# Kernel optimization log

Measured on AMD Instinct MI355X. Metric: run time of the kernel, lower is better.

## Reference

```python
import jax, jax.numpy as jnp
import numpy as np

# Default bone connections from BoneLengthLoss.__init__
BONES = np.array([(1, 2), (1, 3), (1, 4), (2, 5), (3, 6), (11, 12), (11, 13), (12, 14),
                  (13, 14), (14, 15), (15, 16), (16, 17), (12, 18), (18, 20), (20, 22),
                  (13, 19), (19, 21), (21, 23), (16, 24), (16, 25), (24, 26), (25, 26),
                  (24, 27), (27, 29), (29, 31), (25, 28), (28, 30), (30, 32), (17, 33),
                  (33, 34), (34, 35), (35, 36)], dtype=np.int32)
J1 = jnp.asarray(BONES[:, 0])
J2 = jnp.asarray(BONES[:, 1])

BATCH = 524288
NUM_KPTS = 37


def setup_inputs() -> dict:
    key = jax.random.key(0)
    k1, k2, k3 = jax.random.split(key, 3)
    pose_3d_pred = jax.random.normal(k1, (BATCH, NUM_KPTS, 3), dtype=jnp.float32)
    pose_3d_ref = jax.random.normal(k2, (BATCH, NUM_KPTS, 3), dtype=jnp.float32)
    valid_mask = jax.random.randint(k3, (BATCH, NUM_KPTS), 0, 2).astype(jnp.bool_)
    return {"pose_3d_pred": pose_3d_pred, "pose_3d_ref": pose_3d_ref,
            "valid_mask": valid_mask}


def reference(pose_3d_pred, pose_3d_ref, valid_mask):
    # Gather both endpoints of every bone: (B, n_bones, 3)
    pred_vec = pose_3d_pred[:, J2, :] - pose_3d_pred[:, J1, :]
    ref_vec = pose_3d_ref[:, J2, :] - pose_3d_ref[:, J1, :]
    pred_len = jnp.linalg.norm(pred_vec, axis=-1)  # (B, n_bones)
    ref_len = jnp.linalg.norm(ref_vec, axis=-1)    # (B, n_bones)
    # Bone is valid iff both endpoints are valid
    bone_valid = (valid_mask[:, J1] & valid_mask[:, J2]).astype(pred_len.dtype)
    # MSE over all valid (batch, bone) entries == mean over concatenated valid lengths
    sq_err = (pred_len - ref_len) ** 2
    num = jnp.sum(sq_err * bone_valid)
    den = jnp.sum(bone_valid)
    return num / den
```

## Files before the change

### kernel.cpp

```cpp
#include <hip/hip_runtime.h>


#define NKPT   37
#define ROWF   111
#define TROWS  64
#define TF4    1776
#define WF4    444
#define TMB    2368
#define TMW    592
#define WMW    148
#define BLOCK  256
#define WPB    4
#define GRID   1280

constexpr int J1[32] = {1,1,1,2,3,11,11,12,13,14,15,16,12,18,20,13,19,21,16,16,24,25,24,27,29,25,28,30,17,33,34,35};
constexpr int J2[32] = {2,3,4,5,6,12,13,14,14,15,16,17,18,20,22,19,21,23,24,25,26,26,27,29,31,28,30,32,33,34,35,36};

__device__ __forceinline__ void glds16(const void* g, void* l) {
    __builtin_amdgcn_global_load_lds(
        (const __attribute__((address_space(1))) void*)g,
        (__attribute__((address_space(3))) void*)l, 16, 0, 0);
}
__device__ __forceinline__ void glds4(const void* g, void* l) {
    __builtin_amdgcn_global_load_lds(
        (const __attribute__((address_space(1))) void*)g,
        (__attribute__((address_space(3))) void*)l, 4, 0, 0);
}

__global__ void init_detect(const unsigned int* __restrict__ mw,
                            unsigned int* __restrict__ ws) {
    const int tid = threadIdx.x;
    if (tid < 4) ws[tid] = 0u;
    __syncthreads();
    unsigned int local = 0;
    for (int i = tid; i < 1024; i += BLOCK) local |= mw[i] & 0xFFFFFF00u;
    if (__any(local != 0) && (tid & 63) == 0) atomicOr(&ws[2], 1u);
}

template <int G>
__device__ __forceinline__ void do_lens(const float* __restrict__ sp,
                                        float* __restrict__ len) {
#pragma unroll
    for (int k = 0; k < 8; ++k) {
        const int a = J1[G * 8 + k] * 3, b = J2[G * 8 + k] * 3;
        float dx = sp[b] - sp[a];
        float dy = sp[b + 1] - sp[a + 1];
        float dz = sp[b + 2] - sp[a + 2];
        len[k] = __builtin_amdgcn_sqrtf(dx * dx + dy * dy + dz * dz);
    }
}

template <int G>
__device__ __forceinline__ void do_acc(const float* __restrict__ sr,
                                       const unsigned char* __restrict__ sm,
                                       const float* __restrict__ plen,
                                       float& num, unsigned int& den) {
#pragma unroll
    for (int k = 0; k < 8; ++k) {
        const int a = J1[G * 8 + k], b = J2[G * 8 + k];
        const int a3 = a * 3, b3 = b * 3;
        float dx = sr[b3] - sr[a3];
        float dy = sr[b3 + 1] - sr[a3 + 1];
        float dz = sr[b3 + 2] - sr[a3 + 2];
        float rl = __builtin_amdgcn_sqrtf(dx * dx + dy * dy + dz * dz);
        unsigned int v = (unsigned int)(sm[a] & sm[b]);
        float d = plen[k] - rl;
        num += v ? d * d : 0.0f;
        den += v;
    }
}

__global__ __launch_bounds__(BLOCK, 5)
void bone_main(const float* __restrict__ pred, const float* __restrict__ ref,
               const void* __restrict__ mask, int B,
               unsigned int* __restrict__ ws, float* __restrict__ out) {
    __shared__ __align__(16) float4 s_pose[TF4];
    __shared__ __align__(4) unsigned char s_mask[TMB];
    __shared__ float s_rn[WPB];
    __shared__ unsigned int s_rd[WPB];

    const int tid  = threadIdx.x;
    const int wave = tid >> 6;
    const int lane = tid & 63;

    const bool mask_bytes = (ws[2] != 0);
    const int ntiles = B / TROWS;

    const float4* __restrict__ pred4 = (const float4*)pred;
    const float4* __restrict__ ref4  = (const float4*)ref;
    const unsigned int* __restrict__ mw = (const unsigned int*)mask;
    const int* __restrict__ mi = (const int*)mask;

    float4* s_pose_w = s_pose + wave * WF4;
    unsigned int* s_mask_w = (unsigned int*)s_mask;

    const float* sp_row = (const float*)s_pose + lane * ROWF;
    const unsigned char* sm_row = s_mask + lane * NKPT;

    float num = 0.0f;
    unsigned int den = 0u;

    for (int t = blockIdx.x; t < ntiles; t += GRID) {
        const float4* pb = pred4 + (size_t)t * TF4 + wave * WF4;
        const float4* rb = ref4  + (size_t)t * TF4 + wave * WF4;

        glds16(pb + lane,       s_pose_w);
        glds16(pb + 64 + lane,  s_pose_w + 64);
        glds16(pb + 128 + lane, s_pose_w + 128);
        glds16(pb + 192 + lane, s_pose_w + 192);
        glds16(pb + 256 + lane, s_pose_w + 256);
        glds16(pb + 320 + lane, s_pose_w + 320);
        if (lane < WF4 - 384)
            glds16(pb + 384 + lane, s_pose_w + 384);
        if (mask_bytes) {
            const unsigned int* mb = mw + (size_t)t * TMW + wave * WMW;
            glds4(mb + lane,      &s_mask_w[wave * WMW]);
            glds4(mb + 64 + lane, &s_mask_w[wave * WMW + 64]);
            if (lane < WMW - 128)
                glds4(mb + 128 + lane, &s_mask_w[wave * WMW + 128]);
        } else {
            const int* mb = mi + (size_t)t * TMB;
            for (int i = tid; i < TMB; i += BLOCK)
                s_mask[i] = (unsigned char)mb[i];
        }
        __syncthreads();

        float plen[8];
        switch (wave) {
            case 0: do_lens<0>(sp_row, plen); break;
            case 1: do_lens<1>(sp_row, plen); break;
            case 2: do_lens<2>(sp_row, plen); break;
            default: do_lens<3>(sp_row, plen); break;
        }
        __syncthreads();

        glds16(rb + lane,       s_pose_w);
        glds16(rb + 64 + lane,  s_pose_w + 64);
        glds16(rb + 128 + lane, s_pose_w + 128);
        glds16(rb + 192 + lane, s_pose_w + 192);
        glds16(rb + 256 + lane, s_pose_w + 256);
        glds16(rb + 320 + lane, s_pose_w + 320);
        if (lane < WF4 - 384)
            glds16(rb + 384 + lane, s_pose_w + 384);
        __syncthreads();

        switch (wave) {
            case 0: do_acc<0>(sp_row, sm_row, plen, num, den); break;
            case 1: do_acc<1>(sp_row, sm_row, plen, num, den); break;
            case 2: do_acc<2>(sp_row, sm_row, plen, num, den); break;
            default: do_acc<3>(sp_row, sm_row, plen, num, den); break;
        }
        __syncthreads();
    }

#pragma unroll
    for (int off = 32; off > 0; off >>= 1) {
        num += __shfl_down(num, off, 64);
        den += __shfl_down(den, off, 64);
    }
    if (lane == 0) { s_rn[wave] = num; s_rd[wave] = den; }
    __syncthreads();
    if (tid == 0) {
        float n = s_rn[0] + s_rn[1] + s_rn[2] + s_rn[3];
        unsigned int d = s_rd[0] + s_rd[1] + s_rd[2] + s_rd[3];
        atomicAdd((float*)&ws[0], n);
        atomicAdd(&ws[1], d);
        __threadfence();
        unsigned int prev = atomicAdd(&ws[3], 1u);
        if (prev == (unsigned int)(gridDim.x - 1)) {
            float fn = atomicAdd((float*)&ws[0], 0.0f);
            unsigned int fd = atomicAdd(&ws[1], 0u);
            out[0] = fn / (float)fd;
        }
    }
}

extern "C" void kernel_launch(void* const* d_in, const int* in_sizes, int n_in,
                              void* d_out, int out_size, void* d_ws, size_t ws_size,
                              hipStream_t stream) {
    const float* pred = (const float*)d_in[0];
    const float* ref  = (const float*)d_in[1];
    const void*  mask = d_in[2];
    const int n_mask  = in_sizes[2];
    const int B       = n_mask / NKPT;
    unsigned int* ws  = (unsigned int*)d_ws;

    init_detect<<<1, BLOCK, 0, stream>>>((const unsigned int*)mask, ws);
    bone_main<<<GRID, BLOCK, 0, stream>>>(pred, ref, mask, B, ws, (float*)d_out);
}
```

Before: 540.7 us.

## Software-pipeline pred/ref/mask staging with separate LDS buffers and vmcnt waits

Splits the shared pose buffer into separate pred and ref buffers and double-buffers the mask, so the next tile's pred and mask loads are issued while the current tile's ref is consumed. Explicit s_waitcnt vmcnt counts and raw barriers replace __syncthreads, letting in-flight global-to-LDS loads stay outstanding across phases. The grid shrinks to 512 blocks and launch bounds drop to 2 blocks per CU to fit the larger LDS footprint. This trades occupancy for per-block memory-level parallelism, and the hand-counted vmcnt values must match the number of issued loads or correctness breaks.

```diff
diff --git a/kernel.cpp b/kernel.cpp
--- a/kernel.cpp
+++ b/kernel.cpp
@@ -11,10 +11,14 @@
 #define WMW    148
 #define BLOCK  256
 #define WPB    4
-#define GRID   1280
+#define GRID   512
 
 constexpr int J1[32] = {1,1,1,2,3,11,11,12,13,14,15,16,12,18,20,13,19,21,16,16,24,25,24,27,29,25,28,30,17,33,34,35};
 constexpr int J2[32] = {2,3,4,5,6,12,13,14,14,15,16,17,18,20,22,19,21,23,24,25,26,26,27,29,31,28,30,32,33,34,35,36};
+
+#define WAITVM(N)  asm volatile("s_waitcnt vmcnt(" #N ")" ::: "memory")
+#define WAITLGKM() asm volatile("s_waitcnt lgkmcnt(0)" ::: "memory")
+#define BAR()      __builtin_amdgcn_s_barrier()
 
 __device__ __forceinline__ void glds16(const void* g, void* l) {
     __builtin_amdgcn_global_load_lds(
@@ -35,6 +39,20 @@
     unsigned int local = 0;
     for (int i = tid; i < 1024; i += BLOCK) local |= mw[i] & 0xFFFFFF00u;
     if (__any(local != 0) && (tid & 63) == 0) atomicOr(&ws[2], 1u);
+}
+
+__device__ __forceinline__ void stage_pose(const float4* __restrict__ g,
+                                           float4* l, int lane) {
+#pragma unroll
+    for (int k = 0; k < 6; ++k) glds16(g + k * 64 + lane, l + k * 64);
+    if (lane < WF4 - 384) glds16(g + 384 + lane, l + 384);
+}
+
+__device__ __forceinline__ void stage_mask(const unsigned int* __restrict__ mb,
+                                           unsigned int* md, int lane) {
+    glds4(mb + lane, md);
+    glds4(mb + 64 + lane, md + 64);
+    if (lane < WMW - 128) glds4(mb + 128 + lane, md + 128);
 }
 
 template <int G>
@@ -70,12 +88,34 @@
     }
 }
 
-__global__ __launch_bounds__(BLOCK, 5)
+__device__ __forceinline__ void lens_sw(int wave, const float* __restrict__ sp,
+                                        float* __restrict__ plen) {
+    switch (wave) {
+        case 0: do_lens<0>(sp, plen); break;
+        case 1: do_lens<1>(sp, plen); break;
+        case 2: do_lens<2>(sp, plen); break;
+        default: do_lens<3>(sp, plen); break;
+    }
+}
+__device__ __forceinline__ void acc_sw(int wave, const float* __restrict__ sr,
+                                       const unsigned char* __restrict__ sm,
+                                       const float* __restrict__ plen,
+                                       float& num, unsigned int& den) {
+    switch (wave) {
+        case 0: do_acc<0>(sr, sm, plen, num, den); break;
+        case 1: do_acc<1>(sr, sm, plen, num, den); break;
+        case 2: do_acc<2>(sr, sm, plen, num, den); break;
+        default: do_acc<3>(sr, sm, plen, num, den); break;
+    }
+}
+
+__global__ __launch_bounds__(BLOCK, 2)
 void bone_main(const float* __restrict__ pred, const float* __restrict__ ref,
                const void* __restrict__ mask, int B,
                unsigned int* __restrict__ ws, float* __restrict__ out) {
-    __shared__ __align__(16) float4 s_pose[TF4];
-    __shared__ __align__(4) unsigned char s_mask[TMB];
+    __shared__ __align__(16) float4 s_pred[TF4];
+    __shared__ __align__(16) float4 s_ref[TF4];
+    __shared__ __align__(16) unsigned int s_maskw[2][TMW];
     __shared__ float s_rn[WPB];
     __shared__ unsigned int s_rd[WPB];
 
@@ -91,66 +131,62 @@
     const unsigned int* __restrict__ mw = (const unsigned int*)mask;
     const int* __restrict__ mi = (const int*)mask;
 
-    float4* s_pose_w = s_pose + wave * WF4;
-    unsigned int* s_mask_w = (unsigned int*)s_mask;
-
-    const float* sp_row = (const float*)s_pose + lane * ROWF;
-    const unsigned char* sm_row = s_mask + lane * NKPT;
+    float4* s_predw = s_pred + wave * WF4;
+    float4* s_refw  = s_ref  + wave * WF4;
+
+    const float* sp_row = (const float*)s_pred + lane * ROWF;
+    const float* sr_row = (const float*)s_ref  + lane * ROWF;
+    const unsigned char* sm_row0 = (const unsigned char*)s_maskw[0] + lane * NKPT;
+    const unsigned char* sm_row1 = (const unsigned char*)s_maskw[1] + lane * NKPT;
 
     float num = 0.0f;
     unsigned int den = 0u;
 
-    for (int t = blockIdx.x; t < ntiles; t += GRID) {
-        const float4* pb = pred4 + (size_t)t * TF4 + wave * WF4;
-        const float4* rb = ref4  + (size_t)t * TF4 + wave * WF4;
-
-        glds16(pb + lane,       s_pose_w);
-        glds16(pb + 64 + lane,  s_pose_w + 64);
-        glds16(pb + 128 + lane, s_pose_w + 128);
-        glds16(pb + 192 + lane, s_pose_w + 192);
-        glds16(pb + 256 + lane, s_pose_w + 256);
-        glds16(pb + 320 + lane, s_pose_w + 320);
-        if (lane < WF4 - 384)
-            glds16(pb + 384 + lane, s_pose_w + 384);
-        if (mask_bytes) {
-            const unsigned int* mb = mw + (size_t)t * TMW + wave * WMW;
-            glds4(mb + lane,      &s_mask_w[wave * WMW]);
-            glds4(mb + 64 + lane, &s_mask_w[wave * WMW + 64]);
-            if (lane < WMW - 128)
-                glds4(mb + 128 + lane, &s_mask_w[wave * WMW + 128]);
-        } else {
+    if (mask_bytes) {
+        int t = blockIdx.x;
+        int par = 0;
+        if (t < ntiles) {
+            stage_pose(pred4 + (size_t)t * TF4 + wave * WF4, s_predw, lane);
+            stage_mask(mw + (size_t)t * TMW + wave * WMW,
+                       &s_maskw[0][wave * WMW], lane);
+        }
+        for (; t < ntiles; t += GRID) {
+            stage_pose(ref4 + (size_t)t * TF4 + wave * WF4, s_refw, lane);
+            WAITVM(7);
+            BAR();
+            float plen[8];
+            lens_sw(wave, sp_row, plen);
+            WAITLGKM();
+            BAR();
+            const int tn = t + GRID;
+            if (tn < ntiles) {
+                stage_pose(pred4 + (size_t)tn * TF4 + wave * WF4, s_predw, lane);
+                stage_mask(mw + (size_t)tn * TMW + wave * WMW,
+                           &s_maskw[par ^ 1][wave * WMW], lane);
+                WAITVM(10);
+            } else {
+                WAITVM(0);
+            }
+            BAR();
+            acc_sw(wave, sr_row, par ? sm_row1 : sm_row0, plen, num, den);
+            WAITLGKM();
+            BAR();
+            par ^= 1;
+        }
+    } else {
+        for (int t = blockIdx.x; t < ntiles; t += GRID) {
+            stage_pose(pred4 + (size_t)t * TF4 + wave * WF4, s_predw, lane);
+            stage_pose(ref4  + (size_t)t * TF4 + wave * WF4, s_refw,  lane);
+            unsigned char* smb = (unsigned char*)s_maskw[0];
             const int* mb = mi + (size_t)t * TMB;
             for (int i = tid; i < TMB; i += BLOCK)
-                s_mask[i] = (unsigned char)mb[i];
-        }
-        __syncthreads();
-
-        float plen[8];
-        switch (wave) {
-            case 0: do_lens<0>(sp_row, plen); break;
-            case 1: do_lens<1>(sp_row, plen); break;
-            case 2: do_lens<2>(sp_row, plen); break;
-            default: do_lens<3>(sp_row, plen); break;
-        }
-        __syncthreads();
-
-        glds16(rb + lane,       s_pose_w);
-        glds16(rb + 64 + lane,  s_pose_w + 64);
-        glds16(rb + 128 + lane, s_pose_w + 128);
-        glds16(rb + 192 + lane, s_pose_w + 192);
-        glds16(rb + 256 + lane, s_pose_w + 256);
-        glds16(rb + 320 + lane, s_pose_w + 320);
-        if (lane < WF4 - 384)
-            glds16(rb + 384 + lane, s_pose_w + 384);
-        __syncthreads();
-
-        switch (wave) {
-            case 0: do_acc<0>(sp_row, sm_row, plen, num, den); break;
-            case 1: do_acc<1>(sp_row, sm_row, plen, num, den); break;
-            case 2: do_acc<2>(sp_row, sm_row, plen, num, den); break;
-            default: do_acc<3>(sp_row, sm_row, plen, num, den); break;
-        }
-        __syncthreads();
+                smb[i] = (unsigned char)mb[i];
+            __syncthreads();
+            float plen[8];
+            lens_sw(wave, sp_row, plen);
+            acc_sw(wave, sr_row, sm_row0, plen, num, den);
+            __syncthreads();
+        }
     }
 
 #pragma unroll
```

New measurement: 538.7 us. No clear change (-0.4%).

## Register double-buffer pred/ref/mask tiles to overlap global loads with compute

Applied to the files above, without the earlier changes.

Replaces the direct global-to-LDS loads with explicit register staging. Each block holds two tiles in registers while it computes on the one already in LDS, so the loads for the next tile are in flight during compute. Pred and ref now get separate LDS buffers and are processed in one pass, dropping two barriers per tile. The grid shrinks to 512 blocks and launch bounds drop to 2 blocks per SM to make room for the large register footprint. The fallback path handles odd tile counts and int masks; the cost is heavy register pressure and reduced occupancy.

```diff
diff --git a/kernel.cpp b/kernel.cpp
--- a/kernel.cpp
+++ b/kernel.cpp
@@ -11,21 +11,13 @@
 #define WMW    148
 #define BLOCK  256
 #define WPB    4
-#define GRID   1280
+#define GRID   512
 
 constexpr int J1[32] = {1,1,1,2,3,11,11,12,13,14,15,16,12,18,20,13,19,21,16,16,24,25,24,27,29,25,28,30,17,33,34,35};
 constexpr int J2[32] = {2,3,4,5,6,12,13,14,14,15,16,17,18,20,22,19,21,23,24,25,26,26,27,29,31,28,30,32,33,34,35,36};
 
-__device__ __forceinline__ void glds16(const void* g, void* l) {
-    __builtin_amdgcn_global_load_lds(
-        (const __attribute__((address_space(1))) void*)g,
-        (__attribute__((address_space(3))) void*)l, 16, 0, 0);
-}
-__device__ __forceinline__ void glds4(const void* g, void* l) {
-    __builtin_amdgcn_global_load_lds(
-        (const __attribute__((address_space(1))) void*)g,
-        (__attribute__((address_space(3))) void*)l, 4, 0, 0);
-}
+#define LGKM0() asm volatile("s_waitcnt lgkmcnt(0)" ::: "memory")
+#define BAR()   __builtin_amdgcn_s_barrier()
 
 __global__ void init_detect(const unsigned int* __restrict__ mw,
                             unsigned int* __restrict__ ws) {
@@ -37,45 +29,105 @@
     if (__any(local != 0) && (tid & 63) == 0) atomicOr(&ws[2], 1u);
 }
 
+struct RegTile {
+    float4 p0, p1, p2, p3, p4, p5, p6;
+    float4 q0, q1, q2, q3, q4, q5, q6;
+    unsigned int m0, m1, m2;
+};
+
+__device__ __forceinline__ void ld_tile(RegTile& T,
+        const float4* __restrict__ pred4, const float4* __restrict__ ref4,
+        const unsigned int* __restrict__ mw, int t, int wave, int lane) {
+    const float4* pb = pred4 + (size_t)t * TF4 + wave * WF4 + lane;
+    const float4* qb = ref4  + (size_t)t * TF4 + wave * WF4 + lane;
+    const unsigned int* mb = mw + (size_t)t * TMW + wave * WMW + lane;
+    T.p0 = pb[0];   T.q0 = qb[0];
+    T.p1 = pb[64];  T.q1 = qb[64];
+    T.p2 = pb[128]; T.q2 = qb[128];
+    T.p3 = pb[192]; T.q3 = qb[192];
+    T.p4 = pb[256]; T.q4 = qb[256];
+    T.p5 = pb[320]; T.q5 = qb[320];
+    if (lane < WF4 - 384) { T.p6 = pb[384]; T.q6 = qb[384]; }
+    T.m0 = mb[0];
+    T.m1 = mb[64];
+    if (lane < WMW - 128) T.m2 = mb[128];
+}
+
+__device__ __forceinline__ void st_tile(const RegTile& T, float4* sp, float4* sq,
+                                        unsigned int* sm, int lane) {
+    sp[lane]       = T.p0;  sq[lane]       = T.q0;
+    sp[64 + lane]  = T.p1;  sq[64 + lane]  = T.q1;
+    sp[128 + lane] = T.p2;  sq[128 + lane] = T.q2;
+    sp[192 + lane] = T.p3;  sq[192 + lane] = T.q3;
+    sp[256 + lane] = T.p4;  sq[256 + lane] = T.q4;
+    sp[320 + lane] = T.p5;  sq[320 + lane] = T.q5;
+    if (lane < WF4 - 384) { sp[384 + lane] = T.p6; sq[384 + lane] = T.q6; }
+    sm[lane]      = T.m0;
+    sm[64 + lane] = T.m1;
+    if (lane < WMW - 128) sm[128 + lane] = T.m2;
+}
+
+__device__ __forceinline__ void ld_pose(RegTile& T,
+        const float4* __restrict__ pred4, const float4* __restrict__ ref4,
+        int t, int wave, int lane) {
+    const float4* pb = pred4 + (size_t)t * TF4 + wave * WF4 + lane;
+    const float4* qb = ref4  + (size_t)t * TF4 + wave * WF4 + lane;
+    T.p0 = pb[0];   T.q0 = qb[0];
+    T.p1 = pb[64];  T.q1 = qb[64];
+    T.p2 = pb[128]; T.q2 = qb[128];
+    T.p3 = pb[192]; T.q3 = qb[192];
+    T.p4 = pb[256]; T.q4 = qb[256];
+    T.p5 = pb[320]; T.q5 = qb[320];
+    if (lane < WF4 - 384) { T.p6 = pb[384]; T.q6 = qb[384]; }
+}
+__device__ __forceinline__ void st_pose(const RegTile& T, float4* sp, float4* sq,
+                                        int lane) {
+    sp[lane]       = T.p0;  sq[lane]       = T.q0;
+    sp[64 + lane]  = T.p1;  sq[64 + lane]  = T.q1;
+    sp[128 + lane] = T.p2;  sq[128 + lane] = T.q2;
+    sp[192 + lane] = T.p3;  sq[192 + lane] = T.q3;
+    sp[256 + lane] = T.p4;  sq[256 + lane] = T.q4;
+    sp[320 + lane] = T.p5;  sq[320 + lane] = T.q5;
+    if (lane < WF4 - 384) { sp[384 + lane] = T.p6; sq[384 + lane] = T.q6; }
+}
+
 template <int G>
-__device__ __forceinline__ void do_lens(const float* __restrict__ sp,
-                                        float* __restrict__ len) {
-#pragma unroll
-    for (int k = 0; k < 8; ++k) {
-        const int a = J1[G * 8 + k] * 3, b = J2[G * 8 + k] * 3;
-        float dx = sp[b] - sp[a];
-        float dy = sp[b + 1] - sp[a + 1];
-        float dz = sp[b + 2] - sp[a + 2];
-        len[k] = __builtin_amdgcn_sqrtf(dx * dx + dy * dy + dz * dz);
-    }
-}
-
-template <int G>
-__device__ __forceinline__ void do_acc(const float* __restrict__ sr,
-                                       const unsigned char* __restrict__ sm,
-                                       const float* __restrict__ plen,
-                                       float& num, unsigned int& den) {
+__device__ __forceinline__ void do_tile(const float* __restrict__ sp,
+                                        const float* __restrict__ sq,
+                                        const unsigned char* __restrict__ sm,
+                                        float& num, unsigned int& den) {
 #pragma unroll
     for (int k = 0; k < 8; ++k) {
         const int a = J1[G * 8 + k], b = J2[G * 8 + k];
         const int a3 = a * 3, b3 = b * 3;
-        float dx = sr[b3] - sr[a3];
-        float dy = sr[b3 + 1] - sr[a3 + 1];
-        float dz = sr[b3 + 2] - sr[a3 + 2];
-        float rl = __builtin_amdgcn_sqrtf(dx * dx + dy * dy + dz * dz);
+        float pdx = sp[b3] - sp[a3];
+        float pdy = sp[b3 + 1] - sp[a3 + 1];
+        float pdz = sp[b3 + 2] - sp[a3 + 2];
+        float qdx = sq[b3] - sq[a3];
+        float qdy = sq[b3 + 1] - sq[a3 + 1];
+        float qdz = sq[b3 + 2] - sq[a3 + 2];
+        float pl = __builtin_amdgcn_sqrtf(pdx * pdx + pdy * pdy + pdz * pdz);
+        float ql = __builtin_amdgcn_sqrtf(qdx * qdx + qdy * qdy + qdz * qdz);
         unsigned int v = (unsigned int)(sm[a] & sm[b]);
-        float d = plen[k] - rl;
+        float d = pl - ql;
         num += v ? d * d : 0.0f;
         den += v;
     }
 }
 
-__global__ __launch_bounds__(BLOCK, 5)
+#define COMPUTE() do { switch (wave) { \
+    case 0: do_tile<0>(sp_row, sq_row, sm_row, num, den); break; \
+    case 1: do_tile<1>(sp_row, sq_row, sm_row, num, den); break; \
+    case 2: do_tile<2>(sp_row, sq_row, sm_row, num, den); break; \
+    default: do_tile<3>(sp_row, sq_row, sm_row, num, den); break; } } while (0)
+
+__global__ __launch_bounds__(BLOCK, 2)
 void bone_main(const float* __restrict__ pred, const float* __restrict__ ref,
                const void* __restrict__ mask, int B,
                unsigned int* __restrict__ ws, float* __restrict__ out) {
-    __shared__ __align__(16) float4 s_pose[TF4];
-    __shared__ __align__(4) unsigned char s_mask[TMB];
+    __shared__ __align__(16) float4 s_pred[TF4];
+    __shared__ __align__(16) float4 s_ref[TF4];
+    __shared__ __align__(16) unsigned int s_maskw[TMW];
     __shared__ float s_rn[WPB];
     __shared__ unsigned int s_rd[WPB];
 
@@ -91,66 +143,62 @@
     const unsigned int* __restrict__ mw = (const unsigned int*)mask;
     const int* __restrict__ mi = (const int*)mask;
 
-    float4* s_pose_w = s_pose + wave * WF4;
-    unsigned int* s_mask_w = (unsigned int*)s_mask;
-
-    const float* sp_row = (const float*)s_pose + lane * ROWF;
-    const unsigned char* sm_row = s_mask + lane * NKPT;
+    float4* spw = s_pred + wave * WF4;
+    float4* sqw = s_ref  + wave * WF4;
+    unsigned int* smw = s_maskw + wave * WMW;
+
+    const float* sp_row = (const float*)s_pred + lane * ROWF;
+    const float* sq_row = (const float*)s_ref  + lane * ROWF;
+    const unsigned char* sm_row = (const unsigned char*)s_maskw + lane * NKPT;
 
     float num = 0.0f;
     unsigned int den = 0u;
 
-    for (int t = blockIdx.x; t < ntiles; t += GRID) {
-        const float4* pb = pred4 + (size_t)t * TF4 + wave * WF4;
-        const float4* rb = ref4  + (size_t)t * TF4 + wave * WF4;
-
-        glds16(pb + lane,       s_pose_w);
-        glds16(pb + 64 + lane,  s_pose_w + 64);
-        glds16(pb + 128 + lane, s_pose_w + 128);
-        glds16(pb + 192 + lane, s_pose_w + 192);
-        glds16(pb + 256 + lane, s_pose_w + 256);
-        glds16(pb + 320 + lane, s_pose_w + 320);
-        if (lane < WF4 - 384)
-            glds16(pb + 384 + lane, s_pose_w + 384);
-        if (mask_bytes) {
-            const unsigned int* mb = mw + (size_t)t * TMW + wave * WMW;
-            glds4(mb + lane,      &s_mask_w[wave * WMW]);
-            glds4(mb + 64 + lane, &s_mask_w[wave * WMW + 64]);
-            if (lane < WMW - 128)
-                glds4(mb + 128 + lane, &s_mask_w[wave * WMW + 128]);
-        } else {
-            const int* mb = mi + (size_t)t * TMB;
-            for (int i = tid; i < TMB; i += BLOCK)
-                s_mask[i] = (unsigned char)mb[i];
+    const int bid = blockIdx.x;
+    const int ntb = (bid < ntiles) ? (ntiles - bid + GRID - 1) / GRID : 0;
+
+    if (mask_bytes && ntb >= 2 && (ntb & 1) == 0) {
+        RegTile A, B2;
+        ld_tile(A,  pred4, ref4, mw, bid,        wave, lane);
+        ld_tile(B2, pred4, ref4, mw, bid + GRID, wave, lane);
+        st_tile(A, spw, sqw, smw, lane);
+        { int tn = bid + 2 * GRID;
+          if (tn < ntiles) ld_tile(A, pred4, ref4, mw, tn, wave, lane); }
+        LGKM0(); BAR();
+        for (int j = 0; j < ntb; j += 2) {
+            COMPUTE();
+            BAR();
+            st_tile(B2, spw, sqw, smw, lane);
+            { int tn = bid + (j + 3) * GRID;
+              if (tn < ntiles) ld_tile(B2, pred4, ref4, mw, tn, wave, lane); }
+            LGKM0(); BAR();
+            COMPUTE();
+            if (j + 2 < ntb) {
+                BAR();
+                st_tile(A, spw, sqw, smw, lane);
+                { int tn = bid + (j + 4) * GRID;
+                  if (tn < ntiles) ld_tile(A, pred4, ref4, mw, tn, wave, lane); }
+                LGKM0(); BAR();
+            }
         }
-        __syncthreads();
-
-        float plen[8];
-        switch (wave) {
-            case 0: do_lens<0>(sp_row, plen); break;
-            case 1: do_lens<1>(sp_row, plen); break;
-            case 2: do_lens<2>(sp_row, plen); break;
-            default: do_lens<3>(sp_row, plen); break;
+    } else {
+        for (int t = bid; t < ntiles; t += GRID) {
+            RegTile A;
+            ld_pose(A, pred4, ref4, t, wave, lane);
+            st_pose(A, spw, sqw, lane);
+            if (mask_bytes) {
+                for (int i = tid; i < TMW; i += BLOCK)
+                    s_maskw[i] = mw[(size_t)t * TMW + i];
+            } else {
+                unsigned char* smb = (unsigned char*)s_maskw;
+                const int* mb = mi + (size_t)t * TMB;
+                for (int i = tid; i < TMB; i += BLOCK)
+                    smb[i] = (unsigned char)mb[i];
+            }
+            __syncthreads();
+            COMPUTE();
+            __syncthreads();
         }
-        __syncthreads();
-
-        glds16(rb + lane,       s_pose_w);
-        glds16(rb + 64 + lane,  s_pose_w + 64);
-        glds16(rb + 128 + lane, s_pose_w + 128);
-        glds16(rb + 192 + lane, s_pose_w + 192);
-        glds16(rb + 256 + lane, s_pose_w + 256);
-        glds16(rb + 320 + lane, s_pose_w + 320);
-        if (lane < WF4 - 384)
-            glds16(rb + 384 + lane, s_pose_w + 384);
-        __syncthreads();
-
-        switch (wave) {
-            case 0: do_acc<0>(sp_row, sm_row, plen, num, den); break;
-            case 1: do_acc<1>(sp_row, sm_row, plen, num, den); break;
-            case 2: do_acc<2>(sp_row, sm_row, plen, num, den); break;
-            default: do_acc<3>(sp_row, sm_row, plen, num, den); break;
-        }
-        __syncthreads();
     }
 
 #pragma unroll
```

Result: slower. 625.0 us (+15.6%).

## Map one bone per lane over row pairs with per-wave LDS staging

Applied to the files above, without the earlier changes.

Replaces the block-wide 64-row tiles, which used global-to-LDS async loads and four block barriers per tile, with a wave-independent loop. Each wave loads two rows (pred and ref) into private LDS through float2 register loads, and each lane computes one bone for one row. This removes __syncthreads, the large LDS footprint and the wave-divergent per-bone switch, and raises the grid and occupancy target. In exchange, each wave issues many small loads per iteration with little memory-level parallelism, uses partial-lane loads, and depends on wave-synchronous LDS ordering without explicit barriers.

```diff
diff --git a/kernel.cpp b/kernel.cpp
--- a/kernel.cpp
+++ b/kernel.cpp
@@ -3,29 +3,13 @@
 
 #define NKPT   37
 #define ROWF   111
-#define TROWS  64
-#define TF4    1776
-#define WF4    444
-#define TMB    2368
-#define TMW    592
-#define WMW    148
 #define BLOCK  256
 #define WPB    4
-#define GRID   1280
+#define GRID   2048
+#define NWAVES (GRID * WPB)
 
-constexpr int J1[32] = {1,1,1,2,3,11,11,12,13,14,15,16,12,18,20,13,19,21,16,16,24,25,24,27,29,25,28,30,17,33,34,35};
-constexpr int J2[32] = {2,3,4,5,6,12,13,14,14,15,16,17,18,20,22,19,21,23,24,25,26,26,27,29,31,28,30,32,33,34,35,36};
-
-__device__ __forceinline__ void glds16(const void* g, void* l) {
-    __builtin_amdgcn_global_load_lds(
-        (const __attribute__((address_space(1))) void*)g,
-        (__attribute__((address_space(3))) void*)l, 16, 0, 0);
-}
-__device__ __forceinline__ void glds4(const void* g, void* l) {
-    __builtin_amdgcn_global_load_lds(
-        (const __attribute__((address_space(1))) void*)g,
-        (__attribute__((address_space(3))) void*)l, 4, 0, 0);
-}
+__device__ const unsigned char dJ1[32] = {1,1,1,2,3,11,11,12,13,14,15,16,12,18,20,13,19,21,16,16,24,25,24,27,29,25,28,30,17,33,34,35};
+__device__ const unsigned char dJ2[32] = {2,3,4,5,6,12,13,14,14,15,16,17,18,20,22,19,21,23,24,25,26,26,27,29,31,28,30,32,33,34,35,36};
 
 __global__ void init_detect(const unsigned int* __restrict__ mw,
                             unsigned int* __restrict__ ws) {
@@ -37,121 +21,94 @@
     if (__any(local != 0) && (tid & 63) == 0) atomicOr(&ws[2], 1u);
 }
 
-template <int G>
-__device__ __forceinline__ void do_lens(const float* __restrict__ sp,
-                                        float* __restrict__ len) {
-#pragma unroll
-    for (int k = 0; k < 8; ++k) {
-        const int a = J1[G * 8 + k] * 3, b = J2[G * 8 + k] * 3;
-        float dx = sp[b] - sp[a];
-        float dy = sp[b + 1] - sp[a + 1];
-        float dz = sp[b + 2] - sp[a + 2];
-        len[k] = __builtin_amdgcn_sqrtf(dx * dx + dy * dy + dz * dz);
-    }
-}
+template <bool MB>
+__device__ __forceinline__ void stream_pairs(
+        const float2* __restrict__ p2, const float2* __restrict__ q2,
+        const unsigned char* __restrict__ mb8, const int* __restrict__ mi,
+        int npairs, int gw, int lane, int laneB,
+        int o1, int o2, int moff1, int moff2,
+        float* __restrict__ sp, float* __restrict__ sq,
+        float& num, unsigned int& den) {
+    float2* sp2 = (float2*)sp;
+    float2* sq2 = (float2*)sq;
+    for (int pr = gw; pr < npairs; pr += NWAVES) {
+        const float2* pb_ = p2 + (size_t)pr * ROWF;
+        const float2* qb_ = q2 + (size_t)pr * ROWF;
+        float2 a0 = pb_[lane];
+        float2 a1 = pb_[laneB];
+        float2 b0 = qb_[lane];
+        float2 b1 = qb_[laneB];
+        unsigned int m1, m2;
+        if (MB) {
+            const unsigned char* mrow = mb8 + (size_t)pr * (2 * NKPT);
+            m1 = (unsigned int)mrow[moff1];
+            m2 = (unsigned int)mrow[moff2];
+        } else {
+            const int* mrow = mi + (size_t)pr * (2 * NKPT);
+            m1 = ((unsigned int)mrow[moff1]) & 1u;
+            m2 = ((unsigned int)mrow[moff2]) & 1u;
+        }
+        sp2[lane] = a0; sp2[laneB] = a1;
+        sq2[lane] = b0; sq2[laneB] = b1;
 
-template <int G>
-__device__ __forceinline__ void do_acc(const float* __restrict__ sr,
-                                       const unsigned char* __restrict__ sm,
-                                       const float* __restrict__ plen,
-                                       float& num, unsigned int& den) {
-#pragma unroll
-    for (int k = 0; k < 8; ++k) {
-        const int a = J1[G * 8 + k], b = J2[G * 8 + k];
-        const int a3 = a * 3, b3 = b * 3;
-        float dx = sr[b3] - sr[a3];
-        float dy = sr[b3 + 1] - sr[a3 + 1];
-        float dz = sr[b3 + 2] - sr[a3 + 2];
-        float rl = __builtin_amdgcn_sqrtf(dx * dx + dy * dy + dz * dz);
-        unsigned int v = (unsigned int)(sm[a] & sm[b]);
-        float d = plen[k] - rl;
-        num += v ? d * d : 0.0f;
+        float p1x = sp[o1], p1y = sp[o1 + 1], p1z = sp[o1 + 2];
+        float p2x = sp[o2], p2y = sp[o2 + 1], p2z = sp[o2 + 2];
+        float q1x = sq[o1], q1y = sq[o1 + 1], q1z = sq[o1 + 2];
+        float q2x = sq[o2], q2y = sq[o2 + 1], q2z = sq[o2 + 2];
+
+        float pdx = p2x - p1x, pdy = p2y - p1y, pdz = p2z - p1z;
+        float qdx = q2x - q1x, qdy = q2y - q1y, qdz = q2z - q1z;
+        float pl = __builtin_amdgcn_sqrtf(pdx * pdx + pdy * pdy + pdz * pdz);
+        float ql = __builtin_amdgcn_sqrtf(qdx * qdx + qdy * qdy + qdz * qdz);
+        unsigned int v = m1 & m2 & 1u;
+        float dd = pl - ql;
+        num += v ? dd * dd : 0.0f;
         den += v;
     }
 }
 
-__global__ __launch_bounds__(BLOCK, 5)
+__global__ __launch_bounds__(BLOCK, 8)
 void bone_main(const float* __restrict__ pred, const float* __restrict__ ref,
                const void* __restrict__ mask, int B,
                unsigned int* __restrict__ ws, float* __restrict__ out) {
-    __shared__ __align__(16) float4 s_pose[TF4];
-    __shared__ __align__(4) unsigned char s_mask[TMB];
+    __shared__ __align__(16) float s_p[WPB][224];
+    __shared__ __align__(16) float s_q[WPB][224];
     __shared__ float s_rn[WPB];
     __shared__ unsigned int s_rd[WPB];
 
     const int tid  = threadIdx.x;
     const int wave = tid >> 6;
     const int lane = tid & 63;
+    const int laneB = (lane < 47) ? 64 + lane : 110;
+    const int b = lane & 31;
+    const int h = lane >> 5;
+
+    const int j1 = (int)dJ1[b], j2 = (int)dJ2[b];
+    const int o1 = h * ROWF + 3 * j1;
+    const int o2 = h * ROWF + 3 * j2;
+    const int moff1 = h * NKPT + j1;
+    const int moff2 = h * NKPT + j2;
 
     const bool mask_bytes = (ws[2] != 0);
-    const int ntiles = B / TROWS;
+    const int npairs = B >> 1;
+    const int gw = blockIdx.x * WPB + wave;
 
-    const float4* __restrict__ pred4 = (const float4*)pred;
-    const float4* __restrict__ ref4  = (const float4*)ref;
-    const unsigned int* __restrict__ mw = (const unsigned int*)mask;
+    const float2* __restrict__ p2 = (const float2*)pred;
+    const float2* __restrict__ q2 = (const float2*)ref;
+    const unsigned char* __restrict__ mb8 = (const unsigned char*)mask;
     const int* __restrict__ mi = (const int*)mask;
-
-    float4* s_pose_w = s_pose + wave * WF4;
-    unsigned int* s_mask_w = (unsigned int*)s_mask;
-
-    const float* sp_row = (const float*)s_pose + lane * ROWF;
-    const unsigned char* sm_row = s_mask + lane * NKPT;
 
     float num = 0.0f;
     unsigned int den = 0u;
 
-    for (int t = blockIdx.x; t < ntiles; t += GRID) {
-        const float4* pb = pred4 + (size_t)t * TF4 + wave * WF4;
-        const float4* rb = ref4  + (size_t)t * TF4 + wave * WF4;
-
-        glds16(pb + lane,       s_pose_w);
-        glds16(pb + 64 + lane,  s_pose_w + 64);
-        glds16(pb + 128 + lane, s_pose_w + 128);
-        glds16(pb + 192 + lane, s_pose_w + 192);
-        glds16(pb + 256 + lane, s_pose_w + 256);
-        glds16(pb + 320 + lane, s_pose_w + 320);
-        if (lane < WF4 - 384)
-            glds16(pb + 384 + lane, s_pose_w + 384);
-        if (mask_bytes) {
-            const unsigned int* mb = mw + (size_t)t * TMW + wave * WMW;
-            glds4(mb + lane,      &s_mask_w[wave * WMW]);
-            glds4(mb + 64 + lane, &s_mask_w[wave * WMW + 64]);
-            if (lane < WMW - 128)
-                glds4(mb + 128 + lane, &s_mask_w[wave * WMW + 128]);
-        } else {
-            const int* mb = mi + (size_t)t * TMB;
-            for (int i = tid; i < TMB; i += BLOCK)
-                s_mask[i] = (unsigned char)mb[i];
-        }
-        __syncthreads();
-
-        float plen[8];
-        switch (wave) {
-            case 0: do_lens<0>(sp_row, plen); break;
-            case 1: do_lens<1>(sp_row, plen); break;
-            case 2: do_lens<2>(sp_row, plen); break;
-            default: do_lens<3>(sp_row, plen); break;
-        }
-        __syncthreads();
-
-        glds16(rb + lane,       s_pose_w);
-        glds16(rb + 64 + lane,  s_pose_w + 64);
-        glds16(rb + 128 + lane, s_pose_w + 128);
-        glds16(rb + 192 + lane, s_pose_w + 192);
-        glds16(rb + 256 + lane, s_pose_w + 256);
-        glds16(rb + 320 + lane, s_pose_w + 320);
-        if (lane < WF4 - 384)
-            glds16(rb + 384 + lane, s_pose_w + 384);
-        __syncthreads();
-
-        switch (wave) {
-            case 0: do_acc<0>(sp_row, sm_row, plen, num, den); break;
-            case 1: do_acc<1>(sp_row, sm_row, plen, num, den); break;
-            case 2: do_acc<2>(sp_row, sm_row, plen, num, den); break;
-            default: do_acc<3>(sp_row, sm_row, plen, num, den); break;
-        }
-        __syncthreads();
-    }
+    if (mask_bytes)
+        stream_pairs<true>(p2, q2, mb8, mi, npairs, gw, lane, laneB,
+                           o1, o2, moff1, moff2, s_p[wave], s_q[wave],
+                           num, den);
+    else
+        stream_pairs<false>(p2, q2, mb8, mi, npairs, gw, lane, laneB,
+                            o1, o2, moff1, moff2, s_p[wave], s_q[wave],
+                            num, den);
 
 #pragma unroll
     for (int off = 32; off > 0; off >>= 1) {
```

Measured after the change: 582.1 us. 1.08x slower.
